# Performance work log

Hardware: AMD Instinct MI355X
Metric: run time of the kernel (lower is better)

The kernel has to match this reference:

```python
import jax, jax.numpy as jnp
import numpy as np

B, L, D, UNITS = 2, 1024, 256, 32


def setup_inputs() -> dict:
    key = jax.random.key(0)
    k1, k2, k3, k4 = jax.random.split(key, 4)
    inputs = jax.random.normal(k1, (B, L, D), dtype=jnp.float32)
    # glorot-style scaled init for weights
    Wt = jax.random.normal(k2, (D, UNITS), dtype=jnp.float32) * (1.0 / np.sqrt(D))
    Wx = jax.random.normal(k3, (UNITS, D), dtype=jnp.float32) * (1.0 / np.sqrt(D))
    bh = jnp.zeros((UNITS,), dtype=jnp.float32)
    Wa = jax.random.normal(k4, (UNITS, 1), dtype=jnp.float32) * (1.0 / np.sqrt(UNITS))
    ba = jnp.zeros((1,), dtype=jnp.float32)
    return {"inputs": inputs, "Wt": Wt, "Wx": Wx, "bh": bh, "Wa": Wa, "ba": ba}


def reference(inputs, Wt, Wx, bh, Wa, ba):
    # q: [B, L, U], k: [B, L, U]  (Wx is stored (U, D), used transposed)
    q = jnp.einsum('bld,du->blu', inputs, Wt)
    k = jnp.einsum('bld,ud->blu', inputs, Wx)
    # beta: [B, Lq, Lk, U] broadcast-add + tanh (the big intermediate)
    beta = jnp.tanh(q[:, :, None, :] + k[:, None, :, :] + bh)
    # alpha: [B, Lq, Lk]
    alpha = jnp.einsum('bqku,u->bqk', beta, Wa[:, 0]) + ba[0]
    # numerically-stable softmax over keys (last axis)
    a = jax.nn.softmax(alpha, axis=-1)
    # weighted sum of values: [B, L, D]
    c_r = jnp.einsum('bqk,bkd->bqd', a, inputs)
    return c_r
```

## Files before the change

### kernel.cpp

```cpp
#include <hip/hip_runtime.h>
#include <cstdint>
#include <cmath>

#define B_ 2
#define L_ 1024
#define D_ 256
#define U_ 32
#define ROWS_ 2048
#define WBS 280
#define PSTR 1032

typedef __attribute__((ext_vector_type(8))) short short8;
typedef __attribute__((ext_vector_type(4))) float floatx4;

#define OFF_P  0u
#define OFF_XT (OFF_P + 524288u)
#define OFF_WV (OFF_XT + 1048576u)

__device__ __forceinline__ float bf2f(unsigned short u) {
    union { unsigned int i; float f; } v; v.i = ((unsigned int)u) << 16; return v.f;
}
__device__ __forceinline__ unsigned short f2bf(float f) {
    union { float f; unsigned int i; } v; v.f = f;
    unsigned int r = v.i + 0x7FFFu + ((v.i >> 16) & 1u);
    return (unsigned short)(r >> 16);
}
__device__ __forceinline__ unsigned int pack_bf(float a, float b) {
    union { float f; unsigned int i; } ua, ub; ua.f = a; ub.f = b;
    unsigned int ra = ua.i + 0x7FFFu + ((ua.i >> 16) & 1u);
    unsigned int rb = ub.i + 0x7FFFu + ((ub.i >> 16) & 1u);
    return (ra >> 16) | (rb & 0xFFFF0000u);
}

__device__ __forceinline__ int sniff_is_f32(const void* x) {
    const unsigned short* xu = (const unsigned short*)x;
    float f = bf2f(xu[2 * (threadIdx.x & 63)]);
    bool plausible = (f == f) && (fabsf(f) < 1e4f) && (fabsf(f) > 1e-10f);
    unsigned long long m = __ballot(plausible);
    return (__popcll(m) >= 60) ? 0 : 1;
}

__device__ __forceinline__ short8 cvt8(const float* p) {
    float4 fa = *(const float4*)p;
    float4 fb = *(const float4*)(p + 4);
    union { short8 s; unsigned int u[4]; } r;
    r.u[0] = pack_bf(fa.x, fa.y);
    r.u[1] = pack_bf(fa.z, fa.w);
    r.u[2] = pack_bf(fb.x, fb.y);
    r.u[3] = pack_bf(fb.z, fb.w);
    return r.s;
}

__global__ void proj_all(const void* __restrict__ x,  const void* __restrict__ Wt,
                         const void* __restrict__ Wx, const void* __restrict__ bh,
                         const void* __restrict__ Wa,
                         float* __restrict__ P, unsigned short* __restrict__ xT,
                         float* __restrict__ WV) {
    const int t = threadIdx.x;
    const int isf32 = sniff_is_f32(x);
    const int n0 = blockIdx.x * 32;
    const int b  = n0 >> 10;
    const int l0 = n0 & (L_ - 1);
    __shared__ unsigned short wb[64 * WBS];
    __shared__ unsigned short xtile[D_ * 34];

    if (blockIdx.x == 0 && t < U_) {
        float wav = isf32 ? ((const float*)Wa)[t] : bf2f(((const unsigned short*)Wa)[t]);
        WV[t] = -2.0f * wav;
    }

    for (int j = 0; j < 32; ++j) {
        const int i = t + 256 * j;
        unsigned short v = isf32 ? f2bf(((const float*)Wt)[i])
                                 : ((const unsigned short*)Wt)[i];
        wb[(i & 31) * WBS + (i >> 5)] = v;
    }
    for (int j = 0; j < 32; ++j) {
        const int e = t + 256 * j;
        unsigned short v = isf32 ? f2bf(((const float*)Wx)[e])
                                 : ((const unsigned short*)Wx)[e];
        wb[(32 + (e >> 8)) * WBS + (e & 255)] = v;
    }
    __syncthreads();

    const int w    = t >> 6;
    const int lane = t & 63;
    const int mt   = w & 1;
    const int rh   = w >> 1;
    const int m    = lane & 15;
    const int kho  = lane >> 4;
    const int u0   = mt * 32;
    const int row  = n0 + 16 * rh + m;

    floatx4 acc0 = {0,0,0,0}, acc1 = {0,0,0,0};
    #pragma unroll
    for (int k0 = 0; k0 < D_; k0 += 32) {
        const int ks = k0 + kho * 8;
        short8 a0 = *(const short8*)(wb + (u0 + m) * WBS + ks);
        short8 a1 = *(const short8*)(wb + (u0 + 16 + m) * WBS + ks);
        short8 b0;
        if (isf32) b0 = cvt8((const float*)x + (size_t)row * D_ + ks);
        else       b0 = *(const short8*)((const unsigned short*)x + (size_t)row * D_ + ks);
        acc0 = __builtin_amdgcn_mfma_f32_16x16x32_bf16(a0, b0, acc0, 0, 0, 0);
        acc1 = __builtin_amdgcn_mfma_f32_16x16x32_bf16(a1, b0, acc1, 0, 0, 0);
        if (mt == 0) {
            union { short8 s; unsigned short h[8]; } uu; uu.s = b0;
            #pragma unroll
            for (int jj = 0; jj < 8; ++jj)
                xtile[(ks + jj) * 34 + 16 * rh + m] = uu.h[jj];
        }
    }

    const float SC = 2.0f * 1.4426950408889634f;
    const int col = lane & 15;
    const int rb  = (lane >> 4) * 4;
    #pragma unroll
    for (int r = 0; r < 4; ++r) {
        const int ua = u0 + rb + r, ub_ = u0 + 16 + rb + r;
        float bh0 = 0.f, bh1 = 0.f;
        if (mt == 0) {
            bh0 = isf32 ? ((const float*)bh)[rb + r]      : bf2f(((const unsigned short*)bh)[rb + r]);
            bh1 = isf32 ? ((const float*)bh)[16 + rb + r] : bf2f(((const unsigned short*)bh)[16 + rb + r]);
        }
        P[(size_t)ua  * ROWS_ + n0 + 16 * rh + col] = __builtin_amdgcn_exp2f(SC * (acc0[r] + bh0));
        P[(size_t)ub_ * ROWS_ + n0 + 16 * rh + col] = __builtin_amdgcn_exp2f(SC * (acc1[r] + bh1));
    }

    __syncthreads();
    unsigned short* xtb = xT + (size_t)b * (D_ * L_) + l0;
    #pragma unroll
    for (int i = 0; i < 16; ++i) {
        const int idx = t + 256 * i;
        const int d = idx >> 4, wq = idx & 15;
        unsigned int p = *(const unsigned int*)(xtile + d * 34 + 2 * wq);
        *(unsigned int*)(xtb + (size_t)d * L_ + 2 * wq) = p;
    }
}

__global__ __launch_bounds__(512) void alpha_pv(const float* __restrict__ P,
                                                const float* __restrict__ WV,
                                                const void* __restrict__ x,
                                                const unsigned short* __restrict__ xT,
                                                void* __restrict__ out) {
    const int t    = threadIdx.x;
    const int w    = t >> 6;
    const int lane = t & 63;
    const int row  = blockIdx.x * 8 + w;
    const int b    = row >> 10;
    const int isf32 = sniff_is_f32(x);
    __shared__ float EK[16 * 1024];
    __shared__ unsigned short Pl[8 * PSTR];

    const float* Pq  = P + row;
    const float* ekg = P + (size_t)32 * ROWS_ + (size_t)b * L_;

    float eq_l = 0.f, wu_l = 0.f;
    if (lane < U_) {
        eq_l = Pq[(size_t)lane * ROWS_];
        wu_l = WV[lane];
    }

    float alp[16];
    #pragma unroll
    for (int j = 0; j < 16; ++j) alp[j] = 0.f;

    for (int h = 0; h < 2; ++h) {
        __syncthreads();
        #pragma unroll
        for (int j = 0; j < 8; ++j) {
            const int idx = t + 512 * j;
            const int ul = idx >> 8, k4 = idx & 255;
            float4 v = *(const float4*)(ekg + (size_t)(16 * h + ul) * ROWS_ + 4 * k4);
            *(float4*)(EK + ul * 1024 + 4 * k4) = v;
        }
        __syncthreads();

        #pragma unroll 4
        for (int ul = 0; ul < 16; ++ul) {
            const int u = 16 * h + ul;
            const float equ = __shfl(eq_l, u, 64);
            const float wu  = __shfl(wu_l, u, 64);
            const float* kr = EK + ul * 1024 + 4 * lane;
            float4 k0 = *(const float4*)(kr);
            float4 k1 = *(const float4*)(kr + 256);
            float4 k2 = *(const float4*)(kr + 512);
            float4 k3 = *(const float4*)(kr + 768);
            alp[0]  = fmaf(wu, __builtin_amdgcn_rcpf(fmaf(equ, k0.x, 1.f)), alp[0]);
            alp[1]  = fmaf(wu, __builtin_amdgcn_rcpf(fmaf(equ, k0.y, 1.f)), alp[1]);
            alp[2]  = fmaf(wu, __builtin_amdgcn_rcpf(fmaf(equ, k0.z, 1.f)), alp[2]);
            alp[3]  = fmaf(wu, __builtin_amdgcn_rcpf(fmaf(equ, k0.w, 1.f)), alp[3]);
            alp[4]  = fmaf(wu, __builtin_amdgcn_rcpf(fmaf(equ, k1.x, 1.f)), alp[4]);
            alp[5]  = fmaf(wu, __builtin_amdgcn_rcpf(fmaf(equ, k1.y, 1.f)), alp[5]);
            alp[6]  = fmaf(wu, __builtin_amdgcn_rcpf(fmaf(equ, k1.z, 1.f)), alp[6]);
            alp[7]  = fmaf(wu, __builtin_amdgcn_rcpf(fmaf(equ, k1.w, 1.f)), alp[7]);
            alp[8]  = fmaf(wu, __builtin_amdgcn_rcpf(fmaf(equ, k2.x, 1.f)), alp[8]);
            alp[9]  = fmaf(wu, __builtin_amdgcn_rcpf(fmaf(equ, k2.y, 1.f)), alp[9]);
            alp[10] = fmaf(wu, __builtin_amdgcn_rcpf(fmaf(equ, k2.z, 1.f)), alp[10]);
            alp[11] = fmaf(wu, __builtin_amdgcn_rcpf(fmaf(equ, k2.w, 1.f)), alp[11]);
            alp[12] = fmaf(wu, __builtin_amdgcn_rcpf(fmaf(equ, k3.x, 1.f)), alp[12]);
            alp[13] = fmaf(wu, __builtin_amdgcn_rcpf(fmaf(equ, k3.y, 1.f)), alp[13]);
            alp[14] = fmaf(wu, __builtin_amdgcn_rcpf(fmaf(equ, k3.z, 1.f)), alp[14]);
            alp[15] = fmaf(wu, __builtin_amdgcn_rcpf(fmaf(equ, k3.w, 1.f)), alp[15]);
        }
    }

    float amax = alp[0];
    #pragma unroll
    for (int j = 1; j < 16; ++j) amax = fmaxf(amax, alp[j]);
    #pragma unroll
    for (int off = 32; off > 0; off >>= 1) amax = fmaxf(amax, __shfl_xor(amax, off, 64));

    const float L2E = 1.4426950408889634f;
    float s = 0.f;
    #pragma unroll
    for (int j = 0; j < 16; ++j) {
        alp[j] = __builtin_amdgcn_exp2f((alp[j] - amax) * L2E);
        s += alp[j];
    }
    #pragma unroll
    for (int off = 32; off > 0; off >>= 1) s += __shfl_xor(s, off, 64);
    const float rinv = __builtin_amdgcn_rcpf(s);

    #pragma unroll
    for (int jj = 0; jj < 4; ++jj) {
        ushort4 pk;
        pk.x = f2bf(alp[4*jj+0] * rinv);
        pk.y = f2bf(alp[4*jj+1] * rinv);
        pk.z = f2bf(alp[4*jj+2] * rinv);
        pk.w = f2bf(alp[4*jj+3] * rinv);
        *(ushort4*)(Pl + w * PSTR + jj * 256 + 4 * lane) = pk;
    }
    __syncthreads();

    const int m  = lane & 15;
    const int ko = (lane >> 4) * 8;
    const int d0 = w * 32;
    const unsigned short* xb0 = xT + (size_t)b * (D_ * L_) + (size_t)(d0 + m) * L_ + ko;
    const unsigned short* xb1 = xb0 + (size_t)16 * L_;
    const unsigned short* pp  = Pl + (size_t)(m & 7) * PSTR + ko;

    floatx4 acc0 = {0,0,0,0}, acc1 = {0,0,0,0};
    short8 pa = *(const short8*)(pp);
    short8 x0 = *(const short8*)(xb0);
    short8 x1 = *(const short8*)(xb1);
    for (int ks = 32; ks < L_; ks += 32) {
        short8 npa = *(const short8*)(pp + ks);
        short8 nx0 = *(const short8*)(xb0 + ks);
        short8 nx1 = *(const short8*)(xb1 + ks);
        acc0 = __builtin_amdgcn_mfma_f32_16x16x32_bf16(pa, x0, acc0, 0, 0, 0);
        acc1 = __builtin_amdgcn_mfma_f32_16x16x32_bf16(pa, x1, acc1, 0, 0, 0);
        pa = npa; x0 = nx0; x1 = nx1;
    }
    acc0 = __builtin_amdgcn_mfma_f32_16x16x32_bf16(pa, x0, acc0, 0, 0, 0);
    acc1 = __builtin_amdgcn_mfma_f32_16x16x32_bf16(pa, x1, acc1, 0, 0, 0);

    const int col = lane & 15;
    const int rb  = (lane >> 4) * 4;
    const int qi0 = (blockIdx.x * 8) & (L_ - 1);
    const size_t obase = (size_t)b * (L_ * D_) + (size_t)qi0 * D_;
    if (rb < 8) {
        if (isf32) {
            float* ob = (float*)out + obase;
            #pragma unroll
            for (int r = 0; r < 4; ++r) {
                ob[(size_t)(rb + r) * D_ + d0 + col]      = acc0[r];
                ob[(size_t)(rb + r) * D_ + d0 + 16 + col] = acc1[r];
            }
        } else {
            unsigned short* ob = (unsigned short*)out + obase;
            #pragma unroll
            for (int r = 0; r < 4; ++r) {
                ob[(size_t)(rb + r) * D_ + d0 + col]      = f2bf(acc0[r]);
                ob[(size_t)(rb + r) * D_ + d0 + 16 + col] = f2bf(acc1[r]);
            }
        }
    }
}

extern "C" void kernel_launch(void* const* d_in, const int* in_sizes, int n_in,
                              void* d_out, int out_size, void* d_ws, size_t ws_size,
                              hipStream_t stream) {
    const void* x  = d_in[0];
    const void* Wt = d_in[1];
    const void* Wx = d_in[2];
    const void* bh = d_in[3];
    const void* Wa = d_in[4];

    char* ws = (char*)d_ws;
    float*          P   = (float*)(ws + OFF_P);
    unsigned short* xT  = (unsigned short*)(ws + OFF_XT);
    float*          WV  = (float*)(ws + OFF_WV);

    proj_all<<<ROWS_ / 32, 256, 0, stream>>>(x, Wt, Wx, bh, Wa, P, xT, WV);
    alpha_pv<<<ROWS_ / 8, 512, 0, stream>>>(P, WV, x, xT, d_out);
}
```

Before: 112.6 us.

## Read key factors from global directly and split PV matmul along K

Drops the 64KB shared-memory staging of the key factors, so each lane reads its float4 key values straight from global/L2 inside the 32-unit loop, with no block barriers. The P·V MFMA stage is restructured: each warp now covers 64 output columns and half of the key range, and the two K-halves are combined through a small shared buffer before the store. The aim is to cut LDS footprint, raising occupancy, and remove the staging syncs. The cost is extra global/L2 traffic, since every warp re-reads the key rows, plus one more reduction barrier.

```diff
diff --git a/kernel.cpp b/kernel.cpp
--- a/kernel.cpp
+++ b/kernel.cpp
@@ -148,11 +148,11 @@
     const int row  = blockIdx.x * 8 + w;
     const int b    = row >> 10;
     const int isf32 = sniff_is_f32(x);
-    __shared__ float EK[16 * 1024];
     __shared__ unsigned short Pl[8 * PSTR];
-
-    const float* Pq  = P + row;
-    const float* ekg = P + (size_t)32 * ROWS_ + (size_t)b * L_;
+    __shared__ float accb[16 * 256];
+
+    const float* Pq = P + row;
+    const float* kb = P + (size_t)32 * ROWS_ + (size_t)b * L_ + 4 * lane;
 
     float eq_l = 0.f, wu_l = 0.f;
     if (lane < U_) {
@@ -164,44 +164,31 @@
     #pragma unroll
     for (int j = 0; j < 16; ++j) alp[j] = 0.f;
 
-    for (int h = 0; h < 2; ++h) {
-        __syncthreads();
-        #pragma unroll
-        for (int j = 0; j < 8; ++j) {
-            const int idx = t + 512 * j;
-            const int ul = idx >> 8, k4 = idx & 255;
-            float4 v = *(const float4*)(ekg + (size_t)(16 * h + ul) * ROWS_ + 4 * k4);
-            *(float4*)(EK + ul * 1024 + 4 * k4) = v;
-        }
-        __syncthreads();
-
-        #pragma unroll 4
-        for (int ul = 0; ul < 16; ++ul) {
-            const int u = 16 * h + ul;
-            const float equ = __shfl(eq_l, u, 64);
-            const float wu  = __shfl(wu_l, u, 64);
-            const float* kr = EK + ul * 1024 + 4 * lane;
-            float4 k0 = *(const float4*)(kr);
-            float4 k1 = *(const float4*)(kr + 256);
-            float4 k2 = *(const float4*)(kr + 512);
-            float4 k3 = *(const float4*)(kr + 768);
-            alp[0]  = fmaf(wu, __builtin_amdgcn_rcpf(fmaf(equ, k0.x, 1.f)), alp[0]);
-            alp[1]  = fmaf(wu, __builtin_amdgcn_rcpf(fmaf(equ, k0.y, 1.f)), alp[1]);
-            alp[2]  = fmaf(wu, __builtin_amdgcn_rcpf(fmaf(equ, k0.z, 1.f)), alp[2]);
-            alp[3]  = fmaf(wu, __builtin_amdgcn_rcpf(fmaf(equ, k0.w, 1.f)), alp[3]);
-            alp[4]  = fmaf(wu, __builtin_amdgcn_rcpf(fmaf(equ, k1.x, 1.f)), alp[4]);
-            alp[5]  = fmaf(wu, __builtin_amdgcn_rcpf(fmaf(equ, k1.y, 1.f)), alp[5]);
-            alp[6]  = fmaf(wu, __builtin_amdgcn_rcpf(fmaf(equ, k1.z, 1.f)), alp[6]);
-            alp[7]  = fmaf(wu, __builtin_amdgcn_rcpf(fmaf(equ, k1.w, 1.f)), alp[7]);
-            alp[8]  = fmaf(wu, __builtin_amdgcn_rcpf(fmaf(equ, k2.x, 1.f)), alp[8]);
-            alp[9]  = fmaf(wu, __builtin_amdgcn_rcpf(fmaf(equ, k2.y, 1.f)), alp[9]);
-            alp[10] = fmaf(wu, __builtin_amdgcn_rcpf(fmaf(equ, k2.z, 1.f)), alp[10]);
-            alp[11] = fmaf(wu, __builtin_amdgcn_rcpf(fmaf(equ, k2.w, 1.f)), alp[11]);
-            alp[12] = fmaf(wu, __builtin_amdgcn_rcpf(fmaf(equ, k3.x, 1.f)), alp[12]);
-            alp[13] = fmaf(wu, __builtin_amdgcn_rcpf(fmaf(equ, k3.y, 1.f)), alp[13]);
-            alp[14] = fmaf(wu, __builtin_amdgcn_rcpf(fmaf(equ, k3.z, 1.f)), alp[14]);
-            alp[15] = fmaf(wu, __builtin_amdgcn_rcpf(fmaf(equ, k3.w, 1.f)), alp[15]);
-        }
+    #pragma unroll 4
+    for (int u = 0; u < U_; ++u) {
+        const float equ = __shfl(eq_l, u, 64);
+        const float wu  = __shfl(wu_l, u, 64);
+        const float* kr = kb + (size_t)u * ROWS_;
+        float4 k0 = *(const float4*)(kr);
+        float4 k1 = *(const float4*)(kr + 256);
+        float4 k2 = *(const float4*)(kr + 512);
+        float4 k3 = *(const float4*)(kr + 768);
+        alp[0]  = fmaf(wu, __builtin_amdgcn_rcpf(fmaf(equ, k0.x, 1.f)), alp[0]);
+        alp[1]  = fmaf(wu, __builtin_amdgcn_rcpf(fmaf(equ, k0.y, 1.f)), alp[1]);
+        alp[2]  = fmaf(wu, __builtin_amdgcn_rcpf(fmaf(equ, k0.z, 1.f)), alp[2]);
+        alp[3]  = fmaf(wu, __builtin_amdgcn_rcpf(fmaf(equ, k0.w, 1.f)), alp[3]);
+        alp[4]  = fmaf(wu, __builtin_amdgcn_rcpf(fmaf(equ, k1.x, 1.f)), alp[4]);
+        alp[5]  = fmaf(wu, __builtin_amdgcn_rcpf(fmaf(equ, k1.y, 1.f)), alp[5]);
+        alp[6]  = fmaf(wu, __builtin_amdgcn_rcpf(fmaf(equ, k1.z, 1.f)), alp[6]);
+        alp[7]  = fmaf(wu, __builtin_amdgcn_rcpf(fmaf(equ, k1.w, 1.f)), alp[7]);
+        alp[8]  = fmaf(wu, __builtin_amdgcn_rcpf(fmaf(equ, k2.x, 1.f)), alp[8]);
+        alp[9]  = fmaf(wu, __builtin_amdgcn_rcpf(fmaf(equ, k2.y, 1.f)), alp[9]);
+        alp[10] = fmaf(wu, __builtin_amdgcn_rcpf(fmaf(equ, k2.z, 1.f)), alp[10]);
+        alp[11] = fmaf(wu, __builtin_amdgcn_rcpf(fmaf(equ, k2.w, 1.f)), alp[11]);
+        alp[12] = fmaf(wu, __builtin_amdgcn_rcpf(fmaf(equ, k3.x, 1.f)), alp[12]);
+        alp[13] = fmaf(wu, __builtin_amdgcn_rcpf(fmaf(equ, k3.y, 1.f)), alp[13]);
+        alp[14] = fmaf(wu, __builtin_amdgcn_rcpf(fmaf(equ, k3.z, 1.f)), alp[14]);
+        alp[15] = fmaf(wu, __builtin_amdgcn_rcpf(fmaf(equ, k3.w, 1.f)), alp[15]);
     }
 
     float amax = alp[0];
@@ -232,46 +219,78 @@
     }
     __syncthreads();
 
+    const int ds = w & 3;
+    const int kh = w >> 2;
     const int m  = lane & 15;
-    const int ko = (lane >> 4) * 8;
-    const int d0 = w * 32;
-    const unsigned short* xb0 = xT + (size_t)b * (D_ * L_) + (size_t)(d0 + m) * L_ + ko;
-    const unsigned short* xb1 = xb0 + (size_t)16 * L_;
+    const int ko = (lane >> 4) * 8 + kh * 512;
+    const int d0 = ds * 64;
+    const unsigned short* xbb = xT + (size_t)b * (D_ * L_) + (size_t)(d0 + m) * L_ + ko;
+    const unsigned short* xb0 = xbb;
+    const unsigned short* xb1 = xbb + (size_t)16 * L_;
+    const unsigned short* xb2 = xbb + (size_t)32 * L_;
+    const unsigned short* xb3 = xbb + (size_t)48 * L_;
     const unsigned short* pp  = Pl + (size_t)(m & 7) * PSTR + ko;
 
-    floatx4 acc0 = {0,0,0,0}, acc1 = {0,0,0,0};
+    floatx4 acc0 = {0,0,0,0}, acc1 = {0,0,0,0}, acc2 = {0,0,0,0}, acc3 = {0,0,0,0};
     short8 pa = *(const short8*)(pp);
     short8 x0 = *(const short8*)(xb0);
     short8 x1 = *(const short8*)(xb1);
-    for (int ks = 32; ks < L_; ks += 32) {
+    short8 x2 = *(const short8*)(xb2);
+    short8 x3 = *(const short8*)(xb3);
+    for (int ks = 32; ks < 512; ks += 32) {
         short8 npa = *(const short8*)(pp + ks);
         short8 nx0 = *(const short8*)(xb0 + ks);
         short8 nx1 = *(const short8*)(xb1 + ks);
+        short8 nx2 = *(const short8*)(xb2 + ks);
+        short8 nx3 = *(const short8*)(xb3 + ks);
         acc0 = __builtin_amdgcn_mfma_f32_16x16x32_bf16(pa, x0, acc0, 0, 0, 0);
         acc1 = __builtin_amdgcn_mfma_f32_16x16x32_bf16(pa, x1, acc1, 0, 0, 0);
-        pa = npa; x0 = nx0; x1 = nx1;
+        acc2 = __builtin_amdgcn_mfma_f32_16x16x32_bf16(pa, x2, acc2, 0, 0, 0);
+        acc3 = __builtin_amdgcn_mfma_f32_16x16x32_bf16(pa, x3, acc3, 0, 0, 0);
+        pa = npa; x0 = nx0; x1 = nx1; x2 = nx2; x3 = nx3;
     }
     acc0 = __builtin_amdgcn_mfma_f32_16x16x32_bf16(pa, x0, acc0, 0, 0, 0);
     acc1 = __builtin_amdgcn_mfma_f32_16x16x32_bf16(pa, x1, acc1, 0, 0, 0);
-
-    const int col = lane & 15;
-    const int rb  = (lane >> 4) * 4;
-    const int qi0 = (blockIdx.x * 8) & (L_ - 1);
-    const size_t obase = (size_t)b * (L_ * D_) + (size_t)qi0 * D_;
-    if (rb < 8) {
-        if (isf32) {
-            float* ob = (float*)out + obase;
-            #pragma unroll
-            for (int r = 0; r < 4; ++r) {
-                ob[(size_t)(rb + r) * D_ + d0 + col]      = acc0[r];
-                ob[(size_t)(rb + r) * D_ + d0 + 16 + col] = acc1[r];
-            }
-        } else {
-            unsigned short* ob = (unsigned short*)out + obase;
-            #pragma unroll
-            for (int r = 0; r < 4; ++r) {
-                ob[(size_t)(rb + r) * D_ + d0 + col]      = f2bf(acc0[r]);
-                ob[(size_t)(rb + r) * D_ + d0 + 16 + col] = f2bf(acc1[r]);
+    acc2 = __builtin_amdgcn_mfma_f32_16x16x32_bf16(pa, x2, acc2, 0, 0, 0);
+    acc3 = __builtin_amdgcn_mfma_f32_16x16x32_bf16(pa, x3, acc3, 0, 0, 0);
+
+    if (kh == 1) {
+        *(floatx4*)(&accb[(ds * 4 + 0) * 256 + lane * 4]) = acc0;
+        *(floatx4*)(&accb[(ds * 4 + 1) * 256 + lane * 4]) = acc1;
+        *(floatx4*)(&accb[(ds * 4 + 2) * 256 + lane * 4]) = acc2;
+        *(floatx4*)(&accb[(ds * 4 + 3) * 256 + lane * 4]) = acc3;
+    }
+    __syncthreads();
+
+    if (kh == 0) {
+        acc0 += *(const floatx4*)(&accb[(ds * 4 + 0) * 256 + lane * 4]);
+        acc1 += *(const floatx4*)(&accb[(ds * 4 + 1) * 256 + lane * 4]);
+        acc2 += *(const floatx4*)(&accb[(ds * 4 + 2) * 256 + lane * 4]);
+        acc3 += *(const floatx4*)(&accb[(ds * 4 + 3) * 256 + lane * 4]);
+
+        const int col = lane & 15;
+        const int rb  = (lane >> 4) * 4;
+        const int qi0 = (blockIdx.x * 8) & (L_ - 1);
+        const size_t obase = (size_t)b * (L_ * D_) + (size_t)qi0 * D_;
+        if (rb < 8) {
+            if (isf32) {
+                float* ob = (float*)out + obase;
+                #pragma unroll
+                for (int r = 0; r < 4; ++r) {
+                    ob[(size_t)(rb + r) * D_ + d0 + col]      = acc0[r];
+                    ob[(size_t)(rb + r) * D_ + d0 + 16 + col] = acc1[r];
+                    ob[(size_t)(rb + r) * D_ + d0 + 32 + col] = acc2[r];
+                    ob[(size_t)(rb + r) * D_ + d0 + 48 + col] = acc3[r];
+                }
+            } else {
+                unsigned short* ob = (unsigned short*)out + obase;
+                #pragma unroll
+                for (int r = 0; r < 4; ++r) {
+                    ob[(size_t)(rb + r) * D_ + d0 + col]      = f2bf(acc0[r]);
+                    ob[(size_t)(rb + r) * D_ + d0 + 16 + col] = f2bf(acc1[r]);
+                    ob[(size_t)(rb + r) * D_ + d0 + 32 + col] = f2bf(acc2[r]);
+                    ob[(size_t)(rb + r) * D_ + d0 + 48 + col] = f2bf(acc3[r]);
+                }
             }
         }
     }
```

Measured after the change: 112.9 us. No clear change (+0.2%).
